# Optimization experiments

Measured on AMD Instinct MI355X. Metric: run time of the kernel, lower is better.

## Reference

```python
import jax, jax.numpy as jnp
import numpy as np

MAX_SHIFT = 128


def setup_inputs() -> dict:
    key = jax.random.key(0)
    k1, k2 = jax.random.split(key)
    B, T = 128, 4096
    preds = jax.random.normal(k1, (B, T), dtype=jnp.float32)
    labels = jax.random.normal(k2, (B, T), dtype=jnp.float32)
    return {"preds": preds, "labels": labels}


def reference(preds, labels):
    # Pad both signals by max_shift zeros on each side (as in F.pad).
    pad = MAX_SHIFT
    pp = jnp.pad(preds, ((0, 0), (pad, pad)))   # [B, L], L = T + 2*max_shift
    pl = jnp.pad(labels, ((0, 0), (pad, pad)))  # [B, L]
    L = pp.shape[-1]

    # torch.roll(x, shifts=s): out[j] = x[(j - s) mod L]. Build all S circular
    # rolls at once via a gather: idx[s, j] = (j - s) mod L.
    shifts = jnp.arange(-MAX_SHIFT, MAX_SHIFT + 1)          # [S]
    idx = (jnp.arange(L)[None, :] - shifts[:, None]) % L    # [S, L]
    rolled = pp[:, idx]                                     # [B, S, L]

    # Pearson correlation of each rolled preds row against padded labels
    # (equivalent to torch.corrcoef(stack([rolled, labels]))[0, 1]).
    xm = rolled - jnp.mean(rolled, axis=-1, keepdims=True)  # [B, S, L]
    ym = pl - jnp.mean(pl, axis=-1, keepdims=True)          # [B, L]
    cov = jnp.einsum('bsl,bl->bs', xm, ym)                  # [B, S]
    x_norm = jnp.sqrt(jnp.sum(xm * xm, axis=-1))            # [B, S]
    y_norm = jnp.sqrt(jnp.sum(ym * ym, axis=-1))            # [B]
    corr = cov / (x_norm * y_norm[:, None])                 # [B, S]

    # correlations_to_loss (abstract in source) instantiated as the standard
    # choice: 1 - max correlation over shifts; forward returns batch mean.
    loss_per_sample = 1.0 - jnp.max(corr, axis=-1)          # [B]
    return jnp.mean(loss_per_sample)
```

## Files before the change

kernel.cpp:

```cpp
#include <hip/hip_runtime.h>

#define BB   128
#define TT   4096
#define NSH  257
#define PAD  128
#define LTOT 4352.0f
#define PPW  (TT + 256)

__device__ __forceinline__ float wave_sum(float v) {
    #pragma unroll
    for (int m = 32; m; m >>= 1) v += __shfl_xor(v, m, 64);
    return v;
}

extern "C" __global__ __launch_bounds__(1024)
void k_all(const float* __restrict__ preds, const float* __restrict__ labels,
           float* __restrict__ val_ws, unsigned* __restrict__ flag_ws,
           float* __restrict__ out) {
    const int bid = blockIdx.x;
    const int tid = threadIdx.x;
    const int l   = tid & 63;
    const int wv  = tid >> 6;

    if (bid == 0) {
        if (wv != 0) return;
        const int r0 = 2 * l, r1 = r0 + 1;
        for (;;) {
            unsigned f0 = __hip_atomic_load(&flag_ws[r0], __ATOMIC_RELAXED, __HIP_MEMORY_SCOPE_AGENT);
            unsigned f1 = __hip_atomic_load(&flag_ws[r1], __ATOMIC_RELAXED, __HIP_MEMORY_SCOPE_AGENT);
            if (__all((f0 == 1u) && (f1 == 1u))) break;
        }
        __builtin_amdgcn_fence(__ATOMIC_ACQUIRE, "agent");
        float v = __hip_atomic_load(&val_ws[r0], __ATOMIC_RELAXED, __HIP_MEMORY_SCOPE_AGENT)
                + __hip_atomic_load(&val_ws[r1], __ATOMIC_RELAXED, __HIP_MEMORY_SCOPE_AGENT);
        v = wave_sum(v);
        if (l == 0) out[0] = v;
        return;
    }

    __shared__ float pp_s[PPW];
    __shared__ float lab_s[TT];
    __shared__ float cov_s[NSH];
    __shared__ float st_s[4];

    const int b = bid - 1;
    const float* pr = preds  + b * TT;
    const float* lr = labels + b * TT;

    #pragma unroll
    for (int v = tid; v < PPW; v += 1024) {
        int idx = v - PAD;
        pp_s[v] = (idx >= 0 && idx < TT) ? pr[idx] : 0.0f;
    }
    #pragma unroll
    for (int v = tid; v < TT; v += 1024) lab_s[v] = lr[v];
    if (tid < NSH) cov_s[tid] = 0.0f;
    if (tid < 4)   st_s[tid]  = 0.0f;
    __syncthreads();

    const int tq0  = wv * (TT / 16);
    const int boff = 256 - 4 * l;

    float4 prev = *reinterpret_cast<const float4*>(&pp_s[tq0 + boff - 4]);
    float a0 = 0.f, a1 = 0.f, a2 = 0.f, a3 = 0.f;

    #pragma unroll 8
    for (int tq = tq0; tq < tq0 + TT / 16; tq += 4) {
        const float4 lab = *reinterpret_cast<const float4*>(&lab_s[tq]);
        const float4 cur = *reinterpret_cast<const float4*>(&pp_s[tq + boff]);
        a0 += lab.x * cur.x;  a0 += lab.y * cur.y;  a0 += lab.z * cur.z;  a0 += lab.w * cur.w;
        a1 += lab.x * prev.w; a1 += lab.y * cur.x;  a1 += lab.z * cur.y;  a1 += lab.w * cur.z;
        a2 += lab.x * prev.z; a2 += lab.y * prev.w; a2 += lab.z * cur.x;  a2 += lab.w * cur.y;
        a3 += lab.x * prev.y; a3 += lab.y * prev.z; a3 += lab.z * prev.w; a3 += lab.w * cur.x;
        prev = cur;
    }
    atomicAdd(&cov_s[4 * l + 0], a0);
    atomicAdd(&cov_s[4 * l + 1], a1);
    atomicAdd(&cov_s[4 * l + 2], a2);
    atomicAdd(&cov_s[4 * l + 3], a3);

    {
        float e = 0.f, sp = 0.f, spp = 0.f, sl = 0.f, sll = 0.f;
        #pragma unroll
        for (int k = 0; k < 4; ++k) {
            int v   = tid + k * 1024;
            float pv = pp_s[v];
            float lv = lab_s[v];
            float pc = pp_s[v + PAD];
            e  += lv * pv;
            sp += pc; spp += pc * pc;
            sl += lv; sll += lv * lv;
        }
        e  = wave_sum(e);
        sp = wave_sum(sp); spp = wave_sum(spp);
        sl = wave_sum(sl); sll = wave_sum(sll);
        if (l == 0) {
            atomicAdd(&cov_s[256], e);
            atomicAdd(&st_s[0], sp); atomicAdd(&st_s[1], spp);
            atomicAdd(&st_s[2], sl); atomicAdd(&st_s[3], sll);
        }
    }
    __syncthreads();

    if (wv == 0) {
        float Sp = st_s[0], Spp = st_s[1], Sl = st_s[2], Sll = st_s[3];
        float xn2 = Spp - Sp * Sp / LTOT;
        float yn2 = Sll - Sl * Sl / LTOT;
        float inv = rsqrtf(xn2 * yn2);
        float cst = Sp * Sl / LTOT;
        float mx = -1e30f;
        for (int j = l; j < NSH; j += 64)
            mx = fmaxf(mx, (cov_s[j] - cst) * inv);
        #pragma unroll
        for (int m = 32; m; m >>= 1) mx = fmaxf(mx, __shfl_xor(mx, m, 64));
        if (l == 0) {
            __hip_atomic_store(&val_ws[b], (1.0f - mx) * (1.0f / BB),
                               __ATOMIC_RELAXED, __HIP_MEMORY_SCOPE_AGENT);
            __hip_atomic_store(&flag_ws[b], 1u,
                               __ATOMIC_RELEASE, __HIP_MEMORY_SCOPE_AGENT);
        }
    }
}

extern "C" void kernel_launch(void* const* d_in, const int* in_sizes, int n_in,
                              void* d_out, int out_size, void* d_ws, size_t ws_size,
                              hipStream_t stream) {
    const float* preds  = (const float*)d_in[0];
    const float* labels = (const float*)d_in[1];
    float*    out     = (float*)d_out;
    float*    val_ws  = (float*)d_ws;
    unsigned* flag_ws = (unsigned*)(val_ws + BB);

    hipLaunchKernelGGL(k_all, dim3(BB + 1), dim3(1024), 0, stream,
                       preds, labels, val_ws, flag_ws, out);
}
```

Baseline: 72.33 us.

## Split each batch row across two blocks with flag-based partial-sum handoff

Each batch row's time axis is now split into two halves, each handled by its own block, so the grid doubles to 256 worker blocks plus one reducer block. The first-half block publishes its partial covariances and statistics to a global workspace and sets a flag; the second-half block spins on that flag, merges the partials and computes the row's correlation maximum. Shared-memory staging also moves to float4 loads. This is meant to occupy more compute units and halve per-block work, at the cost of an extra inter-block spin-wait and global round trip. It relies on the paired blocks being co-resident so the spin cannot deadlock.

Result: slower. 102.6 us (+41.8%).

```diff
diff --git a/kernel.cpp b/kernel.cpp
--- a/kernel.cpp
+++ b/kernel.cpp
@@ -5,7 +5,9 @@
 #define NSH  257
 #define PAD  128
 #define LTOT 4352.0f
-#define PPW  (TT + 256)
+#define TC   2048
+#define PPW  (TC + 256)
+#define PRW  264
 
 __device__ __forceinline__ float wave_sum(float v) {
     #pragma unroll
@@ -15,6 +17,7 @@
 
 extern "C" __global__ __launch_bounds__(1024)
 void k_all(const float* __restrict__ preds, const float* __restrict__ labels,
+           float* __restrict__ pair_ws, unsigned* __restrict__ pair_flag,
            float* __restrict__ val_ws, unsigned* __restrict__ flag_ws,
            float* __restrict__ out) {
     const int bid = blockIdx.x;
@@ -38,34 +41,41 @@
         return;
     }
 
-    __shared__ float pp_s[PPW];
-    __shared__ float lab_s[TT];
+    __shared__ __align__(16) float pp_s[PPW];
+    __shared__ __align__(16) float lab_s[TC];
     __shared__ float cov_s[NSH];
     __shared__ float st_s[4];
 
-    const int b = bid - 1;
+    const int w  = bid - 1;
+    const int b  = w >> 1;
+    const int c  = w & 1;
+    const int t0 = c * TC;
     const float* pr = preds  + b * TT;
     const float* lr = labels + b * TT;
 
-    #pragma unroll
-    for (int v = tid; v < PPW; v += 1024) {
-        int idx = v - PAD;
-        pp_s[v] = (idx >= 0 && idx < TT) ? pr[idx] : 0.0f;
+    {
+        const float4 zero = {0.f, 0.f, 0.f, 0.f};
+        if (tid < PPW / 4) {
+            int g = t0 - PAD + 4 * tid;
+            *reinterpret_cast<float4*>(&pp_s[4 * tid]) =
+                (g >= 0 && g + 3 < TT) ? *reinterpret_cast<const float4*>(pr + g) : zero;
+        }
+        if (tid < TC / 4)
+            *reinterpret_cast<float4*>(&lab_s[4 * tid]) =
+                *reinterpret_cast<const float4*>(lr + t0 + 4 * tid);
+        if (tid < NSH) cov_s[tid] = 0.0f;
+        if (tid < 4)   st_s[tid]  = 0.0f;
     }
-    #pragma unroll
-    for (int v = tid; v < TT; v += 1024) lab_s[v] = lr[v];
-    if (tid < NSH) cov_s[tid] = 0.0f;
-    if (tid < 4)   st_s[tid]  = 0.0f;
     __syncthreads();
 
-    const int tq0  = wv * (TT / 16);
+    const int tq0  = wv * (TC / 16);
     const int boff = 256 - 4 * l;
 
     float4 prev = *reinterpret_cast<const float4*>(&pp_s[tq0 + boff - 4]);
     float a0 = 0.f, a1 = 0.f, a2 = 0.f, a3 = 0.f;
 
     #pragma unroll 8
-    for (int tq = tq0; tq < tq0 + TT / 16; tq += 4) {
+    for (int tq = tq0; tq < tq0 + TC / 16; tq += 4) {
         const float4 lab = *reinterpret_cast<const float4*>(&lab_s[tq]);
         const float4 cur = *reinterpret_cast<const float4*>(&pp_s[tq + boff]);
         a0 += lab.x * cur.x;  a0 += lab.y * cur.y;  a0 += lab.z * cur.z;  a0 += lab.w * cur.w;
@@ -82,8 +92,8 @@
     {
         float e = 0.f, sp = 0.f, spp = 0.f, sl = 0.f, sll = 0.f;
         #pragma unroll
-        for (int k = 0; k < 4; ++k) {
-            int v   = tid + k * 1024;
+        for (int k = 0; k < 2; ++k) {
+            int v    = tid + k * 1024;
             float pv = pp_s[v];
             float lv = lab_s[v];
             float pc = pp_s[v + PAD];
@@ -100,6 +110,30 @@
             atomicAdd(&st_s[2], sl); atomicAdd(&st_s[3], sll);
         }
     }
+    __syncthreads();
+
+    float* pws = pair_ws + b * PRW;
+
+    if (c == 0) {
+        if (tid < NSH)
+            __hip_atomic_store(&pws[tid], cov_s[tid], __ATOMIC_RELAXED, __HIP_MEMORY_SCOPE_AGENT);
+        if (tid < 4)
+            __hip_atomic_store(&pws[NSH + tid], st_s[tid], __ATOMIC_RELAXED, __HIP_MEMORY_SCOPE_AGENT);
+        __syncthreads();
+        if (tid == 0)
+            __hip_atomic_store(&pair_flag[b], 1u, __ATOMIC_RELEASE, __HIP_MEMORY_SCOPE_AGENT);
+        return;
+    }
+
+    if (tid == 0) {
+        while (__hip_atomic_load(&pair_flag[b], __ATOMIC_RELAXED, __HIP_MEMORY_SCOPE_AGENT) != 1u) {}
+    }
+    __syncthreads();
+    __builtin_amdgcn_fence(__ATOMIC_ACQUIRE, "agent");
+    if (tid < NSH)
+        cov_s[tid] += __hip_atomic_load(&pws[tid], __ATOMIC_RELAXED, __HIP_MEMORY_SCOPE_AGENT);
+    if (tid < 4)
+        st_s[tid]  += __hip_atomic_load(&pws[NSH + tid], __ATOMIC_RELAXED, __HIP_MEMORY_SCOPE_AGENT);
     __syncthreads();
 
     if (wv == 0) {
@@ -127,10 +161,12 @@
                               hipStream_t stream) {
     const float* preds  = (const float*)d_in[0];
     const float* labels = (const float*)d_in[1];
-    float*    out     = (float*)d_out;
-    float*    val_ws  = (float*)d_ws;
-    unsigned* flag_ws = (unsigned*)(val_ws + BB);
+    float*    out       = (float*)d_out;
+    float*    pair_ws   = (float*)d_ws;
+    unsigned* pair_flag = (unsigned*)(pair_ws + BB * PRW);
+    float*    val_ws    = (float*)(pair_flag + BB);
+    unsigned* flag_ws   = (unsigned*)(val_ws + BB);
 
-    hipLaunchKernelGGL(k_all, dim3(BB + 1), dim3(1024), 0, stream,
-                       preds, labels, val_ws, flag_ws, out);
+    hipLaunchKernelGGL(k_all, dim3(2 * BB + 1), dim3(1024), 0, stream,
+                       preds, labels, pair_ws, pair_flag, val_ws, flag_ws, out);
 }
```
